# Performance work log

Hardware: AMD Instinct MI355X
Metric: run time of the kernel (lower is better)

Reference implementation:

```python
import jax, jax.numpy as jnp
import numpy as np
from jax import lax

D_MODEL = 1024
INNER = 2048  # d_model * expansion(2)
K = 3         # depthwise conv kernel size
B, S = 4, 2048


def setup_inputs() -> dict:
    key = jax.random.key(0)
    ks = jax.random.split(key, 8)
    s = 0.02
    return {
        "x": jax.random.normal(ks[0], (B, S, D_MODEL), dtype=jnp.float32),
        "W_in": jax.random.normal(ks[1], (D_MODEL, 2 * INNER), dtype=jnp.float32) * s,
        "b_in": jnp.zeros((2 * INNER,), jnp.float32),
        "conv_w": jax.random.normal(ks[2], (INNER, 1, K), dtype=jnp.float32) * s,
        "conv_b": jnp.zeros((INNER,), jnp.float32),
        "Wa": jax.random.normal(ks[3], (INNER, INNER), dtype=jnp.float32) * s,
        "ba": jnp.zeros((INNER,), jnp.float32),
        "Wb": jax.random.normal(ks[4], (INNER, INNER), dtype=jnp.float32) * s,
        "bb": jnp.zeros((INNER,), jnp.float32),
        "Wc": jax.random.normal(ks[5], (INNER, INNER), dtype=jnp.float32) * s,
        "bc": jnp.zeros((INNER,), jnp.float32),
        "Wo": jax.random.normal(ks[6], (INNER, D_MODEL), dtype=jnp.float32) * s,
        "bo": jnp.zeros((D_MODEL,), jnp.float32),
        "gamma": jnp.ones((D_MODEL,), jnp.float32),
        "beta": jnp.zeros((D_MODEL,), jnp.float32),
    }


def _layernorm(x, gamma, beta, eps=1e-5):
    mu = jnp.mean(x, axis=-1, keepdims=True)
    var = jnp.mean(jnp.square(x - mu), axis=-1, keepdims=True)
    return (x - mu) * lax.rsqrt(var + eps) * gamma + beta


def _forward(x, W_in, b_in, conv_w, conv_b, Wa, ba, Wb, bb, Wc, bc, Wo, bo, gamma, beta):
    residual = x
    xn = _layernorm(x, gamma, beta)
    proj = xn @ W_in + b_in                       # [B,S,2*INNER]
    projected, gate = jnp.split(proj, 2, axis=-1)
    # causal depthwise conv: torch pads K-1 both sides then keeps first S -> left pad K-1
    conv_in = jnp.swapaxes(projected, 1, 2)       # [B,INNER,S]
    conv_out = lax.conv_general_dilated(
        conv_in, conv_w, window_strides=(1,), padding=[(K - 1, 0)],
        feature_group_count=INNER,
        dimension_numbers=("NCH", "OIH", "NCH"))
    conv_out = jnp.swapaxes(conv_out + conv_b[None, :, None], 1, 2)  # [B,S,INNER]
    u = jax.nn.silu(conv_out) * jax.nn.sigmoid(gate)
    a = jax.nn.sigmoid(u @ Wa + ba)
    b = jax.nn.sigmoid(u @ Wb + bb)
    c = jnp.tanh(u @ Wc + bc)

    # linear recurrence over time: state = a_t*state + b_t*u_t; out = c_t*state + u_t
    def step(state, abu):
        a_t, b_t, c_t, u_t = abu
        state = a_t * state + b_t * u_t
        return state, c_t * state + u_t

    seq = tuple(jnp.swapaxes(t, 0, 1) for t in (a, b, c, u))  # [S,B,INNER]
    _, y = lax.scan(step, jnp.zeros((x.shape[0], INNER), x.dtype), seq)
    y = jnp.swapaxes(y, 0, 1)                      # [B,S,INNER]
    return residual + y @ Wo + bo


def reference(x, W_in, b_in, conv_w, conv_b, Wa, ba, Wb, bb, Wc, bc, Wo, bo, gamma, beta):
    return _forward(x, W_in, b_in, conv_w, conv_b, Wa, ba, Wb, bb, Wc, bc, Wo, bo, gamma, beta)
```

## Files before the change

### kernel.cpp

```cpp
#include <hip/hip_runtime.h>
#include <hip/hip_bf16.h>
#include <cstdint>
#include <cstddef>

#define BB 4
#define SS 2048
#define DM 1024
#define INNER 2048
#define CHUNK 64
#define NCHK (SS / CHUNK)

typedef __attribute__((ext_vector_type(8))) __bf16 bf16x8;
typedef __attribute__((ext_vector_type(4))) float f32x4;
typedef __attribute__((ext_vector_type(8))) unsigned short ushort8;
typedef __attribute__((ext_vector_type(4))) unsigned short ushort4v;

#define GPTR(p) ((const __attribute__((address_space(1))) void*)(p))
#define LPTR(p) ((__attribute__((address_space(3))) void*)(p))
#define SB() __builtin_amdgcn_sched_barrier(0)

#define XN_SCALE 8.0f
#define WIN_SCALE 32.0f
#define PROJ_SCALE_INV (1.0f / 256.0f)
#define U_SCALE 128.0f
#define W_SCALE 32.0f
#define ABC_SCALE_INV (1.0f / 4096.0f)
#define Y_SCALE 128.0f
#define WO_SCALE 32.0f
#define WO_SCALE_INV (1.0f / 4096.0f)

__device__ inline float b2f(unsigned short h) {
  union { unsigned u; float f; } v; v.u = ((unsigned)h) << 16; return v.f;
}
__device__ inline unsigned short f2b(float f) {
  unsigned u = __float_as_uint(f);
  u += 0x7fff + ((u >> 16) & 1);
  return (unsigned short)(u >> 16);
}
__device__ inline unsigned pack2(float lo, float hi) {
  return (unsigned)f2b(lo) | ((unsigned)f2b(hi) << 16);
}
__device__ inline unsigned pk_fp8x4(float a, float b, float c, float d) {
  unsigned w = 0;
  w = __builtin_amdgcn_cvt_pk_fp8_f32(a, b, (int)w, 0);
  w = __builtin_amdgcn_cvt_pk_fp8_f32(c, d, (int)w, 1);
  return w;
}
__device__ inline float sigmoidf_(float x) { return 1.0f / (1.0f + __expf(-x)); }
__device__ inline float tanhf_(float x) { return 2.0f / (1.0f + __expf(-2.0f * x)) - 1.0f; }

__global__ void transpose_cast_fp8_kernel(const float* __restrict__ src,
                                          unsigned char* __restrict__ dst,
                                          int R, int C, float scale) {
  __shared__ float tile[32][33];
  const int c0 = blockIdx.x * 32, r0 = blockIdx.y * 32;
  const int tx = threadIdx.x, ty = threadIdx.y;
  #pragma unroll
  for (int j = ty; j < 32; j += 8)
    tile[j][tx] = src[(size_t)(r0 + j) * C + c0 + tx];
  __syncthreads();
  #pragma unroll
  for (int j = ty; j < 32; j += 8) {
    const int w = __builtin_amdgcn_cvt_pk_fp8_f32(tile[tx][j] * scale, 0.f, 0, 0);
    dst[(size_t)(c0 + j) * R + r0 + tx] = (unsigned char)(w & 0xff);
  }
}

__global__ __launch_bounds__(256) void layernorm_kernel(
    const float* __restrict__ x, const float* __restrict__ gamma,
    const float* __restrict__ beta, unsigned char* __restrict__ out) {
  const int row = blockIdx.x;
  const int tid = threadIdx.x;
  const float4 v = *(const float4*)(x + (size_t)row * DM + tid * 4);
  float s = v.x + v.y + v.z + v.w;
  #pragma unroll
  for (int o = 32; o >= 1; o >>= 1) s += __shfl_down(s, o, 64);
  __shared__ float red[8];
  const int wid = tid >> 6, lane = tid & 63;
  if (lane == 0) red[wid] = s;
  __syncthreads();
  const float mu = (red[0] + red[1] + red[2] + red[3]) * (1.f / DM);
  const float d0 = v.x - mu, d1 = v.y - mu, d2 = v.z - mu, d3 = v.w - mu;
  float sq = d0 * d0 + d1 * d1 + d2 * d2 + d3 * d3;
  #pragma unroll
  for (int o = 32; o >= 1; o >>= 1) sq += __shfl_down(sq, o, 64);
  if (lane == 0) red[4 + wid] = sq;
  __syncthreads();
  const float var = (red[4] + red[5] + red[6] + red[7]) * (1.f / DM);
  const float rs = rsqrtf(var + 1e-5f);
  const int c0 = tid * 4;
  const float o0 = (d0 * rs * gamma[c0 + 0] + beta[c0 + 0]) * XN_SCALE;
  const float o1 = (d1 * rs * gamma[c0 + 1] + beta[c0 + 1]) * XN_SCALE;
  const float o2 = (d2 * rs * gamma[c0 + 2] + beta[c0 + 2]) * XN_SCALE;
  const float o3 = (d3 * rs * gamma[c0 + 3] + beta[c0 + 3]) * XN_SCALE;
  *(unsigned*)(out + (size_t)row * DM + c0) = pk_fp8x4(o0, o1, o2, o3);
}

template <int OUTMODE>
__global__ __launch_bounds__(512, 1) void gemm64_fp8(
    const unsigned char* __restrict__ A, const unsigned char* __restrict__ Bt,
    const float* __restrict__ bias, unsigned short* __restrict__ Cout,
    int M, int N, int K, int nbx, float sinv) {
  __shared__ __align__(16) unsigned char lds8[2 * 32768];
  const int tid = threadIdx.x;
  const int nwg = gridDim.x;
  const int cpx = nwg >> 3;
  const int bid = blockIdx.x;
  const int swz = (bid & 7) * cpx + (bid >> 3);
  const int m0 = (swz / nbx) * 256, n0 = (swz % nbx) * 256;

  const int l = tid & 63, w = tid >> 6;
  const int wr = w >> 2, wc = w & 3;
  const int NT = K >> 6;

  const int lane_tail = ((l >> 4) >> 1) * 256 + (l & 15) * 16 + ((l >> 4) & 1) * 8;
  const int a_off = wr * 8192 + lane_tail;
  const int b_off = 16384 + wc * 4096 + lane_tail;

  f32x4 acc[8][4];
  #pragma unroll
  for (int i = 0; i < 8; i++)
    #pragma unroll
    for (int j = 0; j < 4; j++) acc[i][j] = (f32x4){0.f, 0.f, 0.f, 0.f};

  const int ru = ((tid >> 6) << 4) | (tid & 15);
  const int su = (tid >> 4) & 3;
  const unsigned char* Af0 = A + (size_t)(m0 + ru) * K + su * 16;
  const unsigned char* Bf0 = Bt + (size_t)(n0 + ru) * K + su * 16;
  const size_t rs128 = (size_t)128 * K;

  auto stageA = [&](int kt) {
    int ktw = kt; if (ktw >= NT) ktw -= NT;
    const int k0 = ktw << 6;
    const int bo = (kt & 1) * 32768;
    __builtin_amdgcn_global_load_lds(GPTR(Af0 + k0), LPTR(&lds8[bo + tid * 16]), 16, 0, 0);
    __builtin_amdgcn_global_load_lds(GPTR(Af0 + rs128 + k0), LPTR(&lds8[bo + (tid + 512) * 16]), 16, 0, 0);
  };
  auto stageB = [&](int kt) {
    int ktw = kt; if (ktw >= NT) ktw -= NT;
    const int k0 = ktw << 6;
    const int bo = (kt & 1) * 32768 + 16384;
    __builtin_amdgcn_global_load_lds(GPTR(Bf0 + k0), LPTR(&lds8[bo + tid * 16]), 16, 0, 0);
    __builtin_amdgcn_global_load_lds(GPTR(Bf0 + rs128 + k0), LPTR(&lds8[bo + (tid + 512) * 16]), 16, 0, 0);
  };

  stageA(0); stageB(0);

  for (int t = 0; t < NT; t++) {
    const int tbo = (t & 1) * 32768;
    unsigned long long bfA[4], afA[4], afB[4], bfB[4], afC[4], afD[4];

    stageA(t + 1);
    SB();
    asm volatile("s_waitcnt vmcnt(2)" ::: "memory");
    SB();
    __builtin_amdgcn_s_barrier();
    SB();
    #pragma unroll
    for (int nf = 0; nf < 4; nf++)
      bfA[nf] = *(const unsigned long long*)&lds8[tbo + b_off + nf * 1024];
    #pragma unroll
    for (int mf = 0; mf < 4; mf++)
      afA[mf] = *(const unsigned long long*)&lds8[tbo + a_off + mf * 1024];
    SB();
    #pragma unroll
    for (int mf = 0; mf < 4; mf++)
      afB[mf] = *(const unsigned long long*)&lds8[tbo + a_off + (4 + mf) * 1024];
    SB();
    __builtin_amdgcn_s_setprio(1);
    #pragma unroll
    for (int mf = 0; mf < 4; mf++)
      #pragma unroll
      for (int nf = 0; nf < 4; nf++)
        acc[mf][nf] = __builtin_amdgcn_mfma_f32_16x16x32_fp8_fp8(
            (long long)bfA[nf], (long long)afA[mf], acc[mf][nf], 0, 0, 0);
    __builtin_amdgcn_s_setprio(0);
    SB();
    stageB(t + 1);
    SB();
    #pragma unroll
    for (int nf = 0; nf < 4; nf++)
      bfB[nf] = *(const unsigned long long*)&lds8[tbo + b_off + nf * 1024 + 512];
    #pragma unroll
    for (int mf = 0; mf < 4; mf++)
      afC[mf] = *(const unsigned long long*)&lds8[tbo + a_off + mf * 1024 + 512];
    SB();
    __builtin_amdgcn_s_setprio(1);
    #pragma unroll
    for (int mf = 0; mf < 4; mf++)
      #pragma unroll
      for (int nf = 0; nf < 4; nf++)
        acc[4 + mf][nf] = __builtin_amdgcn_mfma_f32_16x16x32_fp8_fp8(
            (long long)bfA[nf], (long long)afB[mf], acc[4 + mf][nf], 0, 0, 0);
    __builtin_amdgcn_s_setprio(0);
    SB();
    #pragma unroll
    for (int mf = 0; mf < 4; mf++)
      afD[mf] = *(const unsigned long long*)&lds8[tbo + a_off + (4 + mf) * 1024 + 512];
    SB();
    __builtin_amdgcn_s_setprio(1);
    #pragma unroll
    for (int mf = 0; mf < 4; mf++)
      #pragma unroll
      for (int nf = 0; nf < 4; nf++)
        acc[mf][nf] = __builtin_amdgcn_mfma_f32_16x16x32_fp8_fp8(
            (long long)bfB[nf], (long long)afC[mf], acc[mf][nf], 0, 0, 0);
    __builtin_amdgcn_s_setprio(0);
    SB();
    __builtin_amdgcn_s_setprio(1);
    #pragma unroll
    for (int mf = 0; mf < 4; mf++)
      #pragma unroll
      for (int nf = 0; nf < 4; nf++)
        acc[4 + mf][nf] = __builtin_amdgcn_mfma_f32_16x16x32_fp8_fp8(
            (long long)bfB[nf], (long long)afD[mf], acc[4 + mf][nf], 0, 0, 0);
    __builtin_amdgcn_s_setprio(0);
    SB();
    __builtin_amdgcn_s_barrier();
    SB();
  }
  asm volatile("s_waitcnt vmcnt(0)" ::: "memory");

  const int rowl = m0 + wr * 128 + (l & 15);
  const int coll = n0 + wc * 64 + (l >> 4) * 4;
  const int seg = (OUTMODE == 2) ? (n0 >> 11) : 0;
  unsigned short* outseg = Cout + (OUTMODE == 2 ? (size_t)seg * M * 2048 : 0);
  #pragma unroll
  for (int mf = 0; mf < 8; mf++) {
    const int row = rowl + mf * 16;
    #pragma unroll
    for (int nf = 0; nf < 4; nf++) {
      const int colb = coll + nf * 16;
      const float4 bv = *(const float4*)(bias + colb);
      float v0 = acc[mf][nf][0] * sinv + bv.x;
      float v1 = acc[mf][nf][1] * sinv + bv.y;
      float v2 = acc[mf][nf][2] * sinv + bv.z;
      float v3 = acc[mf][nf][3] * sinv + bv.w;
      if (OUTMODE == 2) {
        if (seg == 2) {
          v0 = tanhf_(v0); v1 = tanhf_(v1); v2 = tanhf_(v2); v3 = tanhf_(v3);
        } else {
          v0 = sigmoidf_(v0); v1 = sigmoidf_(v1); v2 = sigmoidf_(v2); v3 = sigmoidf_(v3);
        }
        uint2 pk = {pack2(v0, v1), pack2(v2, v3)};
        *(uint2*)(outseg + (size_t)row * 2048 + (colb & 2047)) = pk;
      } else {
        uint2 pk = {pack2(v0, v1), pack2(v2, v3)};
        *(uint2*)(Cout + (size_t)row * N + colb) = pk;
      }
    }
  }
}

__global__ __launch_bounds__(512, 1) void gemm_fp8_wo(
    const unsigned char* __restrict__ A, const unsigned char* __restrict__ Bt,
    const float* __restrict__ bias, float* __restrict__ Cout,
    const float* __restrict__ resid, int M, int N, int K, int nbx) {
  __shared__ __align__(16) unsigned char lds8[2 * 24576];
  const int tid = threadIdx.x;
  const int nwg = gridDim.x;
  const int cpx = nwg >> 3;
  const int bid = blockIdx.x;
  const int swz = (bid & 7) * cpx + (bid >> 3);
  const int m0 = (swz / nbx) * 256, n0 = (swz % nbx) * 128;

  const int l = tid & 63, w = tid >> 6;
  const int wr = w >> 1, wc = w & 1;
  const int NT = K >> 6;

  const int lane_tail = ((l >> 4) >> 1) * 256 + (l & 15) * 16 + ((l >> 4) & 1) * 8;
  const int a_off = wr * 4096 + lane_tail;
  const int b_off = 16384 + wc * 4096 + lane_tail;

  f32x4 acc[4][4];
  #pragma unroll
  for (int i = 0; i < 4; i++)
    #pragma unroll
    for (int j = 0; j < 4; j++) acc[i][j] = (f32x4){0.f, 0.f, 0.f, 0.f};

  const int ru = ((tid >> 6) << 4) | (tid & 15);
  const int su = (tid >> 4) & 3;
  const unsigned char* Af0 = A + (size_t)(m0 + ru) * K + su * 16;
  const unsigned char* Bf0 = Bt + (size_t)(n0 + ru) * K + su * 16;
  const size_t rs128 = (size_t)128 * K;

  auto stageA = [&](int kt) {
    int ktw = kt; if (ktw >= NT) ktw -= NT;
    const int k0 = ktw << 6;
    const int bo = (kt & 1) * 24576;
    __builtin_amdgcn_global_load_lds(GPTR(Af0 + k0), LPTR(&lds8[bo + tid * 16]), 16, 0, 0);
    __builtin_amdgcn_global_load_lds(GPTR(Af0 + rs128 + k0), LPTR(&lds8[bo + (tid + 512) * 16]), 16, 0, 0);
  };
  auto stageB = [&](int kt) {
    int ktw = kt; if (ktw >= NT) ktw -= NT;
    const int k0 = ktw << 6;
    const int bo = (kt & 1) * 24576 + 16384;
    __builtin_amdgcn_global_load_lds(GPTR(Bf0 + k0), LPTR(&lds8[bo + tid * 16]), 16, 0, 0);
  };

  stageA(0); stageB(0);

  for (int t = 0; t < NT; t++) {
    const int tbo = (t & 1) * 24576;
    unsigned long long af[4], bfv[4];

    stageA(t + 1);
    SB();
    asm volatile("s_waitcnt vmcnt(2)" ::: "memory");
    SB();
    __builtin_amdgcn_s_barrier();
    SB();
    #pragma unroll
    for (int nf = 0; nf < 4; nf++)
      bfv[nf] = *(const unsigned long long*)&lds8[tbo + b_off + nf * 1024];
    #pragma unroll
    for (int mf = 0; mf < 4; mf++)
      af[mf] = *(const unsigned long long*)&lds8[tbo + a_off + mf * 1024];
    asm volatile("s_waitcnt lgkmcnt(0)" ::: "memory");
    SB();
    __builtin_amdgcn_s_setprio(1);
    #pragma unroll
    for (int mf = 0; mf < 4; mf++)
      #pragma unroll
      for (int nf = 0; nf < 4; nf++)
        acc[mf][nf] = __builtin_amdgcn_mfma_f32_16x16x32_fp8_fp8(
            (long long)bfv[nf], (long long)af[mf], acc[mf][nf], 0, 0, 0);
    __builtin_amdgcn_s_setprio(0);
    SB();
    stageB(t + 1);
    SB();
    #pragma unroll
    for (int nf = 0; nf < 4; nf++)
      bfv[nf] = *(const unsigned long long*)&lds8[tbo + b_off + nf * 1024 + 512];
    #pragma unroll
    for (int mf = 0; mf < 4; mf++)
      af[mf] = *(const unsigned long long*)&lds8[tbo + a_off + mf * 1024 + 512];
    asm volatile("s_waitcnt lgkmcnt(0)" ::: "memory");
    SB();
    __builtin_amdgcn_s_setprio(1);
    #pragma unroll
    for (int mf = 0; mf < 4; mf++)
      #pragma unroll
      for (int nf = 0; nf < 4; nf++)
        acc[mf][nf] = __builtin_amdgcn_mfma_f32_16x16x32_fp8_fp8(
            (long long)bfv[nf], (long long)af[mf], acc[mf][nf], 0, 0, 0);
    __builtin_amdgcn_s_setprio(0);
    SB();
    __builtin_amdgcn_s_barrier();
    SB();
  }
  asm volatile("s_waitcnt vmcnt(0)" ::: "memory");

  const int rowl = m0 + wr * 64 + (l & 15);
  const int coll = n0 + wc * 64 + (l >> 4) * 4;
  #pragma unroll
  for (int mf = 0; mf < 4; mf++) {
    const int row = rowl + mf * 16;
    #pragma unroll
    for (int nf = 0; nf < 4; nf++) {
      const int colb = coll + nf * 16;
      const float4 bv = *(const float4*)(bias + colb);
      const size_t idx = (size_t)row * N + colb;
      const float4 rv = *(const float4*)(resid + idx);
      float4 ov;
      ov.x = acc[mf][nf][0] * WO_SCALE_INV + bv.x + rv.x;
      ov.y = acc[mf][nf][1] * WO_SCALE_INV + bv.y + rv.y;
      ov.z = acc[mf][nf][2] * WO_SCALE_INV + bv.z + rv.z;
      ov.w = acc[mf][nf][3] * WO_SCALE_INV + bv.w + rv.w;
      *(float4*)(Cout + idx) = ov;
    }
  }
}

__global__ __launch_bounds__(256) void conv_gate_kernel(
    const unsigned short* __restrict__ proj, const float* __restrict__ conv_w,
    const float* __restrict__ conv_b, unsigned short* __restrict__ u,
    unsigned char* __restrict__ u8) {
  const size_t idx = ((size_t)blockIdx.x * 256 + threadIdx.x) * 8;
  const int d = (int)(idx & (INNER - 1));
  const size_t bt = idx >> 11;
  const int t = (int)(bt & (SS - 1));
  const size_t rowbase = bt * (2 * INNER);
  const ushort8 zero = {0, 0, 0, 0, 0, 0, 0, 0};
  ushort8 p0 = *(const ushort8*)(proj + rowbase + d);
  ushort8 p1 = zero, p2 = zero;
  if (t >= 1) p1 = *(const ushort8*)(proj + rowbase - 2 * INNER + d);
  if (t >= 2) p2 = *(const ushort8*)(proj + rowbase - 4 * INNER + d);
  ushort8 g = *(const ushort8*)(proj + rowbase + INNER + d);
  ushort8 res;
  float us[8];
  #pragma unroll
  for (int j = 0; j < 8; j++) {
    const int dj = d + j;
    float sv = conv_b[dj] + conv_w[dj * 3] * b2f(p2[j]) +
               conv_w[dj * 3 + 1] * b2f(p1[j]) + conv_w[dj * 3 + 2] * b2f(p0[j]);
    float uu = sv * sigmoidf_(sv) * sigmoidf_(b2f(g[j]));
    us[j] = uu;
    res[j] = f2b(uu);
  }
  *(ushort8*)(u + idx) = res;
  uint2 pk;
  pk.x = pk_fp8x4(us[0] * U_SCALE, us[1] * U_SCALE, us[2] * U_SCALE, us[3] * U_SCALE);
  pk.y = pk_fp8x4(us[4] * U_SCALE, us[5] * U_SCALE, us[6] * U_SCALE, us[7] * U_SCALE);
  *(uint2*)(u8 + idx) = pk;
}

__global__ __launch_bounds__(256) void scan_phase1(
    const unsigned short* __restrict__ a, const unsigned short* __restrict__ b,
    const unsigned short* __restrict__ u,
    float* __restrict__ P, float* __restrict__ S) {
  const int g = blockIdx.x * 256 + threadIdx.x;
  const int ch = (g & (INNER / 4 - 1)) * 4;
  const int chunk = (g >> 9) & (NCHK - 1);
  const int bb = g >> 14;
  size_t base = ((size_t)bb * SS + (size_t)chunk * CHUNK) * INNER + ch;
  float st0 = 0.f, st1 = 0.f, st2 = 0.f, st3 = 0.f;
  float p0 = 1.f, p1 = 1.f, p2 = 1.f, p3 = 1.f;
  for (int t = 0; t < CHUNK; t++) {
    const ushort4v av = *(const ushort4v*)(a + base);
    const ushort4v bv = *(const ushort4v*)(b + base);
    const ushort4v uv = *(const ushort4v*)(u + base);
    const float a0 = b2f(av[0]), a1 = b2f(av[1]), a2 = b2f(av[2]), a3 = b2f(av[3]);
    st0 = fmaf(a0, st0, b2f(bv[0]) * b2f(uv[0])); p0 *= a0;
    st1 = fmaf(a1, st1, b2f(bv[1]) * b2f(uv[1])); p1 *= a1;
    st2 = fmaf(a2, st2, b2f(bv[2]) * b2f(uv[2])); p2 *= a2;
    st3 = fmaf(a3, st3, b2f(bv[3]) * b2f(uv[3])); p3 *= a3;
    base += INNER;
  }
  const size_t o = ((size_t)bb * NCHK + chunk) * INNER + ch;
  *(float4*)(P + o) = (float4){p0, p1, p2, p3};
  *(float4*)(S + o) = (float4){st0, st1, st2, st3};
}

__global__ __launch_bounds__(256) void scan_phase2(
    const float* __restrict__ P, const float* __restrict__ S,
    float* __restrict__ Carry) {
  const int g = blockIdx.x * 256 + threadIdx.x;
  const int ch = g & (INNER - 1);
  const int bb = g >> 11;
  float carry = 0.f;
  for (int k = 0; k < NCHK; k++) {
    const size_t o = ((size_t)bb * NCHK + k) * INNER + ch;
    Carry[o] = carry;
    carry = fmaf(P[o], carry, S[o]);
  }
}

__global__ __launch_bounds__(256) void scan_phase3(
    const unsigned short* __restrict__ a, const unsigned short* __restrict__ b,
    const unsigned short* __restrict__ c, unsigned short* __restrict__ u,
    unsigned char* __restrict__ y8, const float* __restrict__ Carry) {
  const int g = blockIdx.x * 256 + threadIdx.x;
  const int ch = (g & (INNER / 4 - 1)) * 4;
  const int chunk = (g >> 9) & (NCHK - 1);
  const int bb = g >> 14;
  size_t base = ((size_t)bb * SS + (size_t)chunk * CHUNK) * INNER + ch;
  const size_t o = ((size_t)bb * NCHK + chunk) * INNER + ch;
  const float4 cv = *(const float4*)(Carry + o);
  float st0 = cv.x, st1 = cv.y, st2 = cv.z, st3 = cv.w;
  for (int t = 0; t < CHUNK; t++) {
    const ushort4v av = *(const ushort4v*)(a + base);
    const ushort4v bv = *(const ushort4v*)(b + base);
    const ushort4v ccv = *(const ushort4v*)(c + base);
    const ushort4v uv = *(const ushort4v*)(u + base);
    const float u0 = b2f(uv[0]), u1 = b2f(uv[1]), u2 = b2f(uv[2]), u3 = b2f(uv[3]);
    st0 = fmaf(b2f(av[0]), st0, b2f(bv[0]) * u0);
    st1 = fmaf(b2f(av[1]), st1, b2f(bv[1]) * u1);
    st2 = fmaf(b2f(av[2]), st2, b2f(bv[2]) * u2);
    st3 = fmaf(b2f(av[3]), st3, b2f(bv[3]) * u3);
    const float y0 = fmaf(b2f(ccv[0]), st0, u0);
    const float y1 = fmaf(b2f(ccv[1]), st1, u1);
    const float y2 = fmaf(b2f(ccv[2]), st2, u2);
    const float y3 = fmaf(b2f(ccv[3]), st3, u3);
    ushort4v yv;
    yv[0] = f2b(y0); yv[1] = f2b(y1); yv[2] = f2b(y2); yv[3] = f2b(y3);
    *(ushort4v*)(u + base) = yv;
    *(unsigned*)(y8 + base) = pk_fp8x4(y0 * Y_SCALE, y1 * Y_SCALE,
                                       y2 * Y_SCALE, y3 * Y_SCALE);
    base += INNER;
  }
}

extern "C" void kernel_launch(void* const* d_in, const int* in_sizes, int n_in,
                              void* d_out, int out_size, void* d_ws, size_t ws_size,
                              hipStream_t stream) {
  const float* x      = (const float*)d_in[0];
  const float* W_in   = (const float*)d_in[1];
  const float* b_in   = (const float*)d_in[2];
  const float* conv_w = (const float*)d_in[3];
  const float* conv_b = (const float*)d_in[4];
  const float* Wa     = (const float*)d_in[5];
  const float* ba     = (const float*)d_in[6];
  const float* Wb     = (const float*)d_in[7];
  const float* b_b    = (const float*)d_in[8];
  const float* Wc     = (const float*)d_in[9];
  const float* bc     = (const float*)d_in[10];
  const float* Wo     = (const float*)d_in[11];
  const float* bo     = (const float*)d_in[12];
  const float* gamma  = (const float*)d_in[13];
  const float* beta   = (const float*)d_in[14];
  float* out = (float*)d_out;

  const size_t M = (size_t)BB * SS;
  char* ws = (char*)d_ws;
  size_t off = 0;
  auto alloc = [&](size_t bytes) {
    char* p = ws + off;
    off += (bytes + 255) & ~(size_t)255;
    return p;
  };
  unsigned char*  Win8   = (unsigned char*)alloc((size_t)4096 * 1024);
  unsigned char*  Wabc8  = (unsigned char*)alloc((size_t)6144 * 2048);
  unsigned char*  Wo8    = (unsigned char*)alloc((size_t)1024 * 2048);
  float*          biasABC = (float*)alloc(6144 * 4);
  unsigned char*  xn8   = (unsigned char*)alloc(M * DM);
  unsigned short* uB    = (unsigned short*)alloc(M * INNER * 2);
  unsigned char*  u8B   = (unsigned char*)alloc(M * INNER);
  unsigned short* abc   = (unsigned short*)alloc(3 * M * INNER * 2);
  unsigned short* proj = abc;
  unsigned short* aB = abc;
  unsigned short* bB = abc + M * INNER;
  unsigned short* cB = abc + 2 * M * INNER;
  float* Pbuf  = (float*)alloc((size_t)BB * NCHK * INNER * 4);
  float* Sbuf  = (float*)alloc((size_t)BB * NCHK * INNER * 4);
  float* Carry = (float*)alloc((size_t)BB * NCHK * INNER * 4);

  hipMemcpyAsync(biasABC,        ba,  2048 * 4, hipMemcpyDeviceToDevice, stream);
  hipMemcpyAsync(biasABC + 2048, b_b, 2048 * 4, hipMemcpyDeviceToDevice, stream);
  hipMemcpyAsync(biasABC + 4096, bc,  2048 * 4, hipMemcpyDeviceToDevice, stream);

  const dim3 tb(32, 8);
  transpose_cast_fp8_kernel<<<dim3(128, 32), tb, 0, stream>>>(W_in, Win8, 1024, 4096, WIN_SCALE);
  transpose_cast_fp8_kernel<<<dim3(64, 64), tb, 0, stream>>>(Wa, Wabc8, 2048, 2048, W_SCALE);
  transpose_cast_fp8_kernel<<<dim3(64, 64), tb, 0, stream>>>(Wb, Wabc8 + 2048 * 2048, 2048, 2048, W_SCALE);
  transpose_cast_fp8_kernel<<<dim3(64, 64), tb, 0, stream>>>(Wc, Wabc8 + 2 * 2048 * 2048, 2048, 2048, W_SCALE);
  transpose_cast_fp8_kernel<<<dim3(32, 64), tb, 0, stream>>>(Wo, Wo8, 2048, 1024, WO_SCALE);

  layernorm_kernel<<<M, 256, 0, stream>>>(x, gamma, beta, xn8);

  gemm64_fp8<0><<<dim3(512), 512, 0, stream>>>(
      xn8, Win8, b_in, proj, M, 4096, 1024, 16, PROJ_SCALE_INV);

  conv_gate_kernel<<<(M * INNER) / (256 * 8), 256, 0, stream>>>(
      proj, conv_w, conv_b, uB, u8B);

  gemm64_fp8<2><<<dim3(768), 512, 0, stream>>>(
      u8B, Wabc8, biasABC, abc, M, 6144, 2048, 24, ABC_SCALE_INV);

  scan_phase1<<<256, 256, 0, stream>>>(aB, bB, uB, Pbuf, Sbuf);
  scan_phase2<<<32, 256, 0, stream>>>(Pbuf, Sbuf, Carry);
  scan_phase3<<<256, 256, 0, stream>>>(aB, bB, cB, uB, u8B, Carry);

  gemm_fp8_wo<<<dim3(256), 512, 0, stream>>>(
      u8B, Wo8, bo, out, x, M, 1024, 2048, 8);
}
```

Measured before the change: 408.6 us.

## Switch FP8 GEMMs to MX-scaled 32x32x64 MFMA instructions

Measured after the change: 372.1 us. 1.1x faster.

```diff
diff --git a/kernel.cpp b/kernel.cpp
--- a/kernel.cpp
+++ b/kernel.cpp
@@ -12,12 +12,18 @@
 
 typedef __attribute__((ext_vector_type(8))) __bf16 bf16x8;
 typedef __attribute__((ext_vector_type(4))) float f32x4;
+typedef __attribute__((ext_vector_type(16))) float f32x16;
+typedef __attribute__((ext_vector_type(8))) int i32x8;
+typedef __attribute__((ext_vector_type(4))) int i32x4;
 typedef __attribute__((ext_vector_type(8))) unsigned short ushort8;
 typedef __attribute__((ext_vector_type(4))) unsigned short ushort4v;
 
 #define GPTR(p) ((const __attribute__((address_space(1))) void*)(p))
 #define LPTR(p) ((__attribute__((address_space(3))) void*)(p))
 #define SB() __builtin_amdgcn_sched_barrier(0)
+
+#define MXMFMA(b, a, c) \
+  __builtin_amdgcn_mfma_scale_f32_32x32x64_f8f6f4((b), (a), (c), 0, 0, 0, 0x7f7f7f7f, 0, 0x7f7f7f7f)
 
 #define XN_SCALE 8.0f
 #define WIN_SCALE 32.0f
@@ -48,6 +54,15 @@
 }
 __device__ inline float sigmoidf_(float x) { return 1.0f / (1.0f + __expf(-x)); }
 __device__ inline float tanhf_(float x) { return 2.0f / (1.0f + __expf(-2.0f * x)) - 1.0f; }
+
+__device__ inline i32x8 ld32(const unsigned char* p) {
+  i32x4 lo = *(const i32x4*)p;
+  i32x4 hi = *(const i32x4*)(p + 256);
+  i32x8 r;
+  r[0] = lo[0]; r[1] = lo[1]; r[2] = lo[2]; r[3] = lo[3];
+  r[4] = hi[0]; r[5] = hi[1]; r[6] = hi[2]; r[7] = hi[3];
+  return r;
+}
 
 __global__ void transpose_cast_fp8_kernel(const float* __restrict__ src,
                                           unsigned char* __restrict__ dst,
@@ -97,7 +112,7 @@
 }
 
 template <int OUTMODE>
-__global__ __launch_bounds__(512, 1) void gemm64_fp8(
+__global__ __launch_bounds__(512, 1) void gemm_mx(
     const unsigned char* __restrict__ A, const unsigned char* __restrict__ Bt,
     const float* __restrict__ bias, unsigned short* __restrict__ Cout,
     int M, int N, int K, int nbx, float sinv) {
@@ -113,15 +128,20 @@
   const int wr = w >> 2, wc = w & 3;
   const int NT = K >> 6;
 
-  const int lane_tail = ((l >> 4) >> 1) * 256 + (l & 15) * 16 + ((l >> 4) & 1) * 8;
-  const int a_off = wr * 8192 + lane_tail;
-  const int b_off = 16384 + wc * 4096 + lane_tail;
-
-  f32x4 acc[8][4];
-  #pragma unroll
-  for (int i = 0; i < 8; i++)
+  const int lane_a = ((l >> 4) & 1) * 1024 + (l >> 5) * 512 + (l & 15) * 16;
+  const int a_base = wr * 8192 + lane_a;
+  const int b_base = 16384 + wc * 4096 + lane_a;
+
+  f32x16 acc[4][2];
+  {
+    f32x16 z;
     #pragma unroll
-    for (int j = 0; j < 4; j++) acc[i][j] = (f32x4){0.f, 0.f, 0.f, 0.f};
+    for (int e = 0; e < 16; e++) z[e] = 0.f;
+    #pragma unroll
+    for (int i = 0; i < 4; i++)
+      #pragma unroll
+      for (int j = 0; j < 2; j++) acc[i][j] = z;
+  }
 
   const int ru = ((tid >> 6) << 4) | (tid & 15);
   const int su = (tid >> 4) & 3;
@@ -148,7 +168,7 @@
 
   for (int t = 0; t < NT; t++) {
     const int tbo = (t & 1) * 32768;
-    unsigned long long bfA[4], afA[4], afB[4], bfB[4], afC[4], afD[4];
+    i32x8 bf0, bf1, af0, af1, af2, af3;
 
     stageA(t + 1);
     SB();
@@ -156,103 +176,71 @@
     SB();
     __builtin_amdgcn_s_barrier();
     SB();
-    #pragma unroll
-    for (int nf = 0; nf < 4; nf++)
-      bfA[nf] = *(const unsigned long long*)&lds8[tbo + b_off + nf * 1024];
-    #pragma unroll
-    for (int mf = 0; mf < 4; mf++)
-      afA[mf] = *(const unsigned long long*)&lds8[tbo + a_off + mf * 1024];
-    SB();
-    #pragma unroll
-    for (int mf = 0; mf < 4; mf++)
-      afB[mf] = *(const unsigned long long*)&lds8[tbo + a_off + (4 + mf) * 1024];
+    bf0 = ld32(&lds8[tbo + b_base]);
+    bf1 = ld32(&lds8[tbo + b_base + 2048]);
+    af0 = ld32(&lds8[tbo + a_base]);
+    af1 = ld32(&lds8[tbo + a_base + 2048]);
     SB();
     __builtin_amdgcn_s_setprio(1);
-    #pragma unroll
-    for (int mf = 0; mf < 4; mf++)
-      #pragma unroll
-      for (int nf = 0; nf < 4; nf++)
-        acc[mf][nf] = __builtin_amdgcn_mfma_f32_16x16x32_fp8_fp8(
-            (long long)bfA[nf], (long long)afA[mf], acc[mf][nf], 0, 0, 0);
+    acc[0][0] = MXMFMA(bf0, af0, acc[0][0]);
+    acc[0][1] = MXMFMA(bf1, af0, acc[0][1]);
+    acc[1][0] = MXMFMA(bf0, af1, acc[1][0]);
+    acc[1][1] = MXMFMA(bf1, af1, acc[1][1]);
     __builtin_amdgcn_s_setprio(0);
     SB();
     stageB(t + 1);
     SB();
-    #pragma unroll
-    for (int nf = 0; nf < 4; nf++)
-      bfB[nf] = *(const unsigned long long*)&lds8[tbo + b_off + nf * 1024 + 512];
-    #pragma unroll
-    for (int mf = 0; mf < 4; mf++)
-      afC[mf] = *(const unsigned long long*)&lds8[tbo + a_off + mf * 1024 + 512];
+    af2 = ld32(&lds8[tbo + a_base + 2 * 2048]);
+    af3 = ld32(&lds8[tbo + a_base + 3 * 2048]);
     SB();
     __builtin_amdgcn_s_setprio(1);
-    #pragma unroll
-    for (int mf = 0; mf < 4; mf++)
-      #pragma unroll
-      for (int nf = 0; nf < 4; nf++)
-        acc[4 + mf][nf] = __builtin_amdgcn_mfma_f32_16x16x32_fp8_fp8(
-            (long long)bfA[nf], (long long)afB[mf], acc[4 + mf][nf], 0, 0, 0);
+    acc[2][0] = MXMFMA(bf0, af2, acc[2][0]);
+    acc[2][1] = MXMFMA(bf1, af2, acc[2][1]);
+    acc[3][0] = MXMFMA(bf0, af3, acc[3][0]);
+    acc[3][1] = MXMFMA(bf1, af3, acc[3][1]);
     __builtin_amdgcn_s_setprio(0);
     SB();
-    #pragma unroll
-    for (int mf = 0; mf < 4; mf++)
-      afD[mf] = *(const unsigned long long*)&lds8[tbo + a_off + (4 + mf) * 1024 + 512];
-    SB();
-    __builtin_amdgcn_s_setprio(1);
-    #pragma unroll
-    for (int mf = 0; mf < 4; mf++)
-      #pragma unroll
-      for (int nf = 0; nf < 4; nf++)
-        acc[mf][nf] = __builtin_amdgcn_mfma_f32_16x16x32_fp8_fp8(
-            (long long)bfB[nf], (long long)afC[mf], acc[mf][nf], 0, 0, 0);
-    __builtin_amdgcn_s_setprio(0);
-    SB();
-    __builtin_amdgcn_s_setprio(1);
-    #pragma unroll
-    for (int mf = 0; mf < 4; mf++)
-      #pragma unroll
-      for (int nf = 0; nf < 4; nf++)
-        acc[4 + mf][nf] = __builtin_amdgcn_mfma_f32_16x16x32_fp8_fp8(
-            (long long)bfB[nf], (long long)afD[mf], acc[4 + mf][nf], 0, 0, 0);
-    __builtin_amdgcn_s_setprio(0);
-    SB();
     __builtin_amdgcn_s_barrier();
     SB();
   }
   asm volatile("s_waitcnt vmcnt(0)" ::: "memory");
 
-  const int rowl = m0 + wr * 128 + (l & 15);
-  const int coll = n0 + wc * 64 + (l >> 4) * 4;
+  const int rowl = m0 + wr * 128 + (l & 31);
+  const int colg = 4 * (l >> 5);
   const int seg = (OUTMODE == 2) ? (n0 >> 11) : 0;
   unsigned short* outseg = Cout + (OUTMODE == 2 ? (size_t)seg * M * 2048 : 0);
   #pragma unroll
-  for (int mf = 0; mf < 8; mf++) {
-    const int row = rowl + mf * 16;
+  for (int mf = 0; mf < 4; mf++) {
+    const int row = rowl + mf * 32;
     #pragma unroll
-    for (int nf = 0; nf < 4; nf++) {
-      const int colb = coll + nf * 16;
-      const float4 bv = *(const float4*)(bias + colb);
-      float v0 = acc[mf][nf][0] * sinv + bv.x;
-      float v1 = acc[mf][nf][1] * sinv + bv.y;
-      float v2 = acc[mf][nf][2] * sinv + bv.z;
-      float v3 = acc[mf][nf][3] * sinv + bv.w;
-      if (OUTMODE == 2) {
-        if (seg == 2) {
-          v0 = tanhf_(v0); v1 = tanhf_(v1); v2 = tanhf_(v2); v3 = tanhf_(v3);
+    for (int nf = 0; nf < 2; nf++) {
+      const int nb = n0 + wc * 64 + nf * 32 + colg;
+      #pragma unroll
+      for (int g = 0; g < 4; g++) {
+        const int col = nb + g * 8;
+        const float4 bv = *(const float4*)(bias + col);
+        float v0 = acc[mf][nf][g * 4 + 0] * sinv + bv.x;
+        float v1 = acc[mf][nf][g * 4 + 1] * sinv + bv.y;
+        float v2 = acc[mf][nf][g * 4 + 2] * sinv + bv.z;
+        float v3 = acc[mf][nf][g * 4 + 3] * sinv + bv.w;
+        if (OUTMODE == 2) {
+          if (seg == 2) {
+            v0 = tanhf_(v0); v1 = tanhf_(v1); v2 = tanhf_(v2); v3 = tanhf_(v3);
+          } else {
+            v0 = sigmoidf_(v0); v1 = sigmoidf_(v1); v2 = sigmoidf_(v2); v3 = sigmoidf_(v3);
+          }
+          uint2 pk = {pack2(v0, v1), pack2(v2, v3)};
+          *(uint2*)(outseg + (size_t)row * 2048 + (col & 2047)) = pk;
         } else {
-          v0 = sigmoidf_(v0); v1 = sigmoidf_(v1); v2 = sigmoidf_(v2); v3 = sigmoidf_(v3);
+          uint2 pk = {pack2(v0, v1), pack2(v2, v3)};
+          *(uint2*)(Cout + (size_t)row * N + col) = pk;
         }
-        uint2 pk = {pack2(v0, v1), pack2(v2, v3)};
-        *(uint2*)(outseg + (size_t)row * 2048 + (colb & 2047)) = pk;
-      } else {
-        uint2 pk = {pack2(v0, v1), pack2(v2, v3)};
-        *(uint2*)(Cout + (size_t)row * N + colb) = pk;
       }
     }
   }
 }
 
-__global__ __launch_bounds__(512, 1) void gemm_fp8_wo(
+__global__ __launch_bounds__(512, 1) void gemm_mx_wo(
     const unsigned char* __restrict__ A, const unsigned char* __restrict__ Bt,
     const float* __restrict__ bias, float* __restrict__ Cout,
     const float* __restrict__ resid, int M, int N, int K, int nbx) {
@@ -268,15 +256,17 @@
   const int wr = w >> 1, wc = w & 1;
   const int NT = K >> 6;
 
-  const int lane_tail = ((l >> 4) >> 1) * 256 + (l & 15) * 16 + ((l >> 4) & 1) * 8;
-  const int a_off = wr * 4096 + lane_tail;
-  const int b_off = 16384 + wc * 4096 + lane_tail;
-
-  f32x4 acc[4][4];
-  #pragma unroll
-  for (int i = 0; i < 4; i++)
+  const int lane_a = ((l >> 4) & 1) * 1024 + (l >> 5) * 512 + (l & 15) * 16;
+  const int a_base = wr * 4096 + lane_a;
+  const int b_base = 16384 + wc * 4096 + lane_a;
+
+  f32x16 acc[2][2];
+  {
+    f32x16 z;
     #pragma unroll
-    for (int j = 0; j < 4; j++) acc[i][j] = (f32x4){0.f, 0.f, 0.f, 0.f};
+    for (int e = 0; e < 16; e++) z[e] = 0.f;
+    acc[0][0] = z; acc[0][1] = z; acc[1][0] = z; acc[1][1] = z;
+  }
 
   const int ru = ((tid >> 6) << 4) | (tid & 15);
   const int su = (tid >> 4) & 3;
@@ -302,7 +292,7 @@
 
   for (int t = 0; t < NT; t++) {
     const int tbo = (t & 1) * 24576;
-    unsigned long long af[4], bfv[4];
+    i32x8 bf0, bf1, af0, af1;
 
     stageA(t + 1);
     SB();
@@ -310,64 +300,50 @@
     SB();
     __builtin_amdgcn_s_barrier();
     SB();
+    bf0 = ld32(&lds8[tbo + b_base]);
+    bf1 = ld32(&lds8[tbo + b_base + 2048]);
+    af0 = ld32(&lds8[tbo + a_base]);
+    SB();
+    __builtin_amdgcn_s_setprio(1);
+    acc[0][0] = MXMFMA(bf0, af0, acc[0][0]);
+    acc[0][1] = MXMFMA(bf1, af0, acc[0][1]);
+    __builtin_amdgcn_s_setprio(0);
+    SB();
+    stageB(t + 1);
+    SB();
+    af1 = ld32(&lds8[tbo + a_base + 2048]);
+    SB();
+    __builtin_amdgcn_s_setprio(1);
+    acc[1][0] = MXMFMA(bf0, af1, acc[1][0]);
+    acc[1][1] = MXMFMA(bf1, af1, acc[1][1]);
+    __builtin_amdgcn_s_setprio(0);
+    SB();
+    __builtin_amdgcn_s_barrier();
+    SB();
+  }
+  asm volatile("s_waitcnt vmcnt(0)" ::: "memory");
+
+  const int rowl = m0 + wr * 64 + (l & 31);
+  const int colg = 4 * (l >> 5);
+  #pragma unroll
+  for (int mf = 0; mf < 2; mf++) {
+    const int row = rowl + mf * 32;
     #pragma unroll
-    for (int nf = 0; nf < 4; nf++)
-      bfv[nf] = *(const unsigned long long*)&lds8[tbo + b_off + nf * 1024];
-    #pragma unroll
-    for (int mf = 0; mf < 4; mf++)
-      af[mf] = *(const unsigned long long*)&lds8[tbo + a_off + mf * 1024];
-    asm volatile("s_waitcnt lgkmcnt(0)" ::: "memory");
-    SB();
-    __builtin_amdgcn_s_setprio(1);
-    #pragma unroll
-    for (int mf = 0; mf < 4; mf++)
+    for (int nf = 0; nf < 2; nf++) {
+      const int nb = n0 + wc * 64 + nf * 32 + colg;
       #pragma unroll
-      for (int nf = 0; nf < 4; nf++)
-        acc[mf][nf] = __builtin_amdgcn_mfma_f32_16x16x32_fp8_fp8(
-            (long long)bfv[nf], (long long)af[mf], acc[mf][nf], 0, 0, 0);
-    __builtin_amdgcn_s_setprio(0);
-    SB();
-    stageB(t + 1);
-    SB();
-    #pragma unroll
-    for (int nf = 0; nf < 4; nf++)
-      bfv[nf] = *(const unsigned long long*)&lds8[tbo + b_off + nf * 1024 + 512];
-    #pragma unroll
-    for (int mf = 0; mf < 4; mf++)
-      af[mf] = *(const unsigned long long*)&lds8[tbo + a_off + mf * 1024 + 512];
-    asm volatile("s_waitcnt lgkmcnt(0)" ::: "memory");
-    SB();
-    __builtin_amdgcn_s_setprio(1);
-    #pragma unroll
-    for (int mf = 0; mf < 4; mf++)
-      #pragma unroll
-      for (int nf = 0; nf < 4; nf++)
-        acc[mf][nf] = __builtin_amdgcn_mfma_f32_16x16x32_fp8_fp8(
-            (long long)bfv[nf], (long long)af[mf], acc[mf][nf], 0, 0, 0);
-    __builtin_amdgcn_s_setprio(0);
-    SB();
-    __builtin_amdgcn_s_barrier();
-    SB();
-  }
-  asm volatile("s_waitcnt vmcnt(0)" ::: "memory");
-
-  const int rowl = m0 + wr * 64 + (l & 15);
-  const int coll = n0 + wc * 64 + (l >> 4) * 4;
-  #pragma unroll
-  for (int mf = 0; mf < 4; mf++) {
-    const int row = rowl + mf * 16;
-    #pragma unroll
-    for (int nf = 0; nf < 4; nf++) {
-      const int colb = coll + nf * 16;
-      const float4 bv = *(const float4*)(bias + colb);
-      const size_t idx = (size_t)row * N + colb;
-      const float4 rv = *(const float4*)(resid + idx);
-      float4 ov;
-      ov.x = acc[mf][nf][0] * WO_SCALE_INV + bv.x + rv.x;
-      ov.y = acc[mf][nf][1] * WO_SCALE_INV + bv.y + rv.y;
-      ov.z = acc[mf][nf][2] * WO_SCALE_INV + bv.z + rv.z;
-      ov.w = acc[mf][nf][3] * WO_SCALE_INV + bv.w + rv.w;
-      *(float4*)(Cout + idx) = ov;
+      for (int g = 0; g < 4; g++) {
+        const int col = nb + g * 8;
+        const float4 bv = *(const float4*)(bias + col);
+        const size_t idx = (size_t)row * N + col;
+        const float4 rv = *(const float4*)(resid + idx);
+        float4 ov;
+        ov.x = acc[mf][nf][g * 4 + 0] * WO_SCALE_INV + bv.x + rv.x;
+        ov.y = acc[mf][nf][g * 4 + 1] * WO_SCALE_INV + bv.y + rv.y;
+        ov.z = acc[mf][nf][g * 4 + 2] * WO_SCALE_INV + bv.z + rv.z;
+        ov.w = acc[mf][nf][g * 4 + 3] * WO_SCALE_INV + bv.w + rv.w;
+        *(float4*)(Cout + idx) = ov;
+      }
     }
   }
 }
@@ -538,19 +514,19 @@
 
   layernorm_kernel<<<M, 256, 0, stream>>>(x, gamma, beta, xn8);
 
-  gemm64_fp8<0><<<dim3(512), 512, 0, stream>>>(
+  gemm_mx<0><<<dim3(512), 512, 0, stream>>>(
       xn8, Win8, b_in, proj, M, 4096, 1024, 16, PROJ_SCALE_INV);
 
   conv_gate_kernel<<<(M * INNER) / (256 * 8), 256, 0, stream>>>(
       proj, conv_w, conv_b, uB, u8B);
 
-  gemm64_fp8<2><<<dim3(768), 512, 0, stream>>>(
+  gemm_mx<2><<<dim3(768), 512, 0, stream>>>(
       u8B, Wabc8, biasABC, abc, M, 6144, 2048, 24, ABC_SCALE_INV);
 
   scan_phase1<<<256, 256, 0, stream>>>(aB, bB, uB, Pbuf, Sbuf);
   scan_phase2<<<32, 256, 0, stream>>>(Pbuf, Sbuf, Carry);
   scan_phase3<<<256, 256, 0, stream>>>(aB, bB, cB, uB, u8B, Carry);
 
-  gemm_fp8_wo<<<dim3(256), 512, 0, stream>>>(
+  gemm_mx_wo<<<dim3(256), 512, 0, stream>>>(
       u8B, Wo8, bo, out, x, M, 1024, 2048, 8);
 }
```
